# Kernel optimization log

Hardware: AMD Instinct MI355X
Metric: run time of the kernel (lower is better)

Reference implementation:

```python
import jax, jax.numpy as jnp
import numpy as np

EPS = 1e-8
N_CLASSES = 11


def _instance_loss(views_1, views_2, masks, labels):
    # views_*: [1, C, H, W]; masks: [1, K, H, W] binary; labels: [1, K] in [0,11)
    C = views_1.shape[1]
    X1 = views_1[0].reshape(C, -1)                      # [C, P]
    X2 = views_2[0].reshape(C, -1)                      # [C, P]
    K = masks.shape[1]
    M = (masks[0].reshape(K, -1) == 1).astype(X1.dtype) # [K, P]
    lab = labels[0]                                     # [K]

    counts = M.sum(axis=1)                              # [K] pixels per instance
    cnt = jnp.maximum(counts, 1.0)

    # per-instance mean feature vector over masked view-1 pixels
    per_chan_sum = M @ X1.T                             # [K, C]
    means = per_chan_sum / cnt[:, None]                 # [K, C]

    # torch.std over ALL elements of the gathered [N_k, C] block (unbiased)
    n_elem = counts * C                                 # [K]
    sum_all = per_chan_sum.sum(axis=1)                  # [K]
    mean_all = sum_all / jnp.maximum(n_elem, 1.0)
    sumsq = M @ (X1 * X1).sum(axis=0)                   # [K]
    var = (sumsq - n_elem * mean_all * mean_all) / jnp.maximum(n_elem - 1.0, 1.0)
    std = jnp.sqrt(jnp.maximum(var, 0.0))               # [K]

    # pairwise mean cosine sim: sim[i,j] = mean_{p in mask_j} cos(means[i], X2[:,p])
    norm_m = jnp.sqrt((means * means).sum(axis=1))      # [K]
    norm_2 = jnp.sqrt((X2 * X2).sum(axis=0))            # [P]
    D = means @ X2                                      # [K, P]
    ratio = D / jnp.maximum(norm_m[:, None] * norm_2[None, :], EPS)
    sim = (ratio @ M.T) / cnt[None, :]                  # [K, K]

    same = lab[:, None] == lab[None, :]
    eye = jnp.eye(K, dtype=bool)

    instance_sim = jnp.zeros(N_CLASSES, X1.dtype).at[lab].add(jnp.diagonal(sim))
    class_sim = jnp.zeros(N_CLASSES, X1.dtype).at[lab].add(
        jnp.where(same & ~eye, sim, 0.0).sum(axis=1))
    class_std = jnp.zeros(N_CLASSES, X1.dtype).at[lab].add(std)

    # negative-pair buckets: human={1,2}, 4wheel={3..8}, 2wheel={9,10}
    g_hum_4w = (lab >= 1) & (lab <= 8)                  # human or 4wheel
    g_4w_2w = (lab >= 3) & (lab <= 10)                  # 4wheel or 2wheel
    g_hum_2w = ((lab >= 1) & (lab <= 2)) | ((lab >= 9) & (lab <= 10))
    diff = ~same

    def neg_bucket(g):
        pair = diff & g[:, None] & g[None, :]
        c = pair.sum().astype(X1.dtype)
        s = jnp.where(pair, sim, 0.0).sum()
        return jnp.where(c > 1, s / c, s).reshape(1)

    neg_4w_hum = neg_bucket(g_hum_4w)
    neg_4w_2w = neg_bucket(g_4w_2w)
    neg_hum_2w = neg_bucket(g_hum_2w)

    class_counts = jnp.zeros(N_CLASSES, X1.dtype).at[lab].add(1.0)
    many = class_counts > 1
    instance_sim = jnp.where(many, instance_sim / jnp.maximum(class_counts, 1.0), instance_sim)
    class_sim = jnp.where(
        many, class_sim / jnp.maximum(class_counts * (class_counts - 1.0), 1.0), class_sim)
    class_std = jnp.where(many, class_std / jnp.maximum(class_counts, 1.0), class_std)

    return instance_sim, class_sim, neg_4w_hum, neg_4w_2w, neg_hum_2w, class_std


def setup_inputs() -> dict:
    key = jax.random.key(0)
    k1, k2, k3, k4 = jax.random.split(key, 4)
    views_1 = jax.random.normal(k1, (1, 64, 512, 512), dtype=jnp.float32)
    views_2 = jax.random.normal(k2, (1, 64, 512, 512), dtype=jnp.float32)
    masks = jax.random.randint(k3, (1, 16, 512, 512), 0, 2, dtype=jnp.int32)
    labels = jax.random.randint(k4, (1, 16), 0, 11, dtype=jnp.int32)
    return {"views_1": views_1, "views_2": views_2, "masks": masks, "labels": labels}


def reference(views_1, views_2, masks, labels):
    return _instance_loss(views_1, views_2, masks, labels)
```

## Files before the change

kernel.cpp:

```cpp
#include <hip/hip_runtime.h>

#define PIX 262144
#define CCH 64
#define KK  16

typedef __attribute__((ext_vector_type(8))) short short8;
typedef __attribute__((ext_vector_type(4))) float f32x4;

__device__ __forceinline__ float wred64(float v) {
    #pragma unroll
    for (int o = 32; o > 0; o >>= 1) v += __shfl_xor(v, o, 64);
    return v;
}

__global__ __launch_bounds__(256) void k2_all(
        const float* __restrict__ x1, const float* __restrict__ x2,
        const int* __restrict__ masks, float* __restrict__ counts_s,
        float* __restrict__ psum_c, float* __restrict__ psumsq_c,
        float* __restrict__ G_c) {
    __shared__ float ylds[128][4];
    int b = blockIdx.x;
    bool TB = (b >= 2048);
    if (TB) b -= 2048;
    int lane = threadIdx.x & 63;
    int wv   = threadIdx.x >> 6;
    int quad = lane >> 4;
    int n    = lane & 15;
    int ch   = wv * 16 + n;
    int base = b * 128;
    int cp   = b & 31;

    const float* Xrow = (TB ? x2 : x1) + (size_t)ch * PIX;
    const int*   Mrow = masks + (size_t)n * PIX;

    int4 mk[8]; float4 xa[4], xb[4];
    #pragma unroll
    for (int i = 0; i < 4; ++i) {
        int kof = base + i * 32 + (quad << 3);
        mk[2*i]   = *(const int4*)(Mrow + kof);
        mk[2*i+1] = *(const int4*)(Mrow + kof + 4);
        xa[i] = *(const float4*)(Xrow + kof);
        xb[i] = *(const float4*)(Xrow + kof + 4);
    }

    float xs[4][8], sq[4][8];
    #pragma unroll
    for (int i = 0; i < 4; ++i) {
        xs[i][0]=xa[i].x; xs[i][1]=xa[i].y; xs[i][2]=xa[i].z; xs[i][3]=xa[i].w;
        xs[i][4]=xb[i].x; xs[i][5]=xb[i].y; xs[i][6]=xb[i].z; xs[i][7]=xb[i].w;
        #pragma unroll
        for (int j = 0; j < 8; ++j) sq[i][j] = xs[i][j] * xs[i][j];
    }

    if (TB) {
        #pragma unroll
        for (int off = 1; off < 16; off <<= 1)
            #pragma unroll
            for (int i = 0; i < 4; ++i)
                #pragma unroll
                for (int j = 0; j < 8; ++j)
                    sq[i][j] += __shfl_xor(sq[i][j], off, 64);
        if (n == 0) {
            #pragma unroll
            for (int i = 0; i < 4; ++i)
                #pragma unroll
                for (int j = 0; j < 8; ++j)
                    ylds[i * 32 + (quad << 3) + j][wv] = sq[i][j];
        }
        __syncthreads();
        #pragma unroll
        for (int i = 0; i < 4; ++i)
            #pragma unroll
            for (int j = 0; j < 8; ++j) {
                float4 v = *(const float4*)ylds[i * 32 + (quad << 3) + j];
                float s = v.x + v.y + v.z + v.w;
                float y = (s > 0.f) ? rsqrtf(s) : 0.f;
                xs[i][j] *= y;
            }
    } else if (wv == 0) {
        int cnt = 0;
        #pragma unroll
        for (int i = 0; i < 8; ++i) {
            cnt += (mk[i].x == 1) + (mk[i].y == 1) + (mk[i].z == 1) + (mk[i].w == 1);
        }
        float fc = (float)cnt;
        fc += __shfl_xor(fc, 16, 64);
        fc += __shfl_xor(fc, 32, 64);
        if (quad == 0) atomicAdd(counts_s + n * 32 + cp, fc);
    }

    f32x4 acc0 = {0.f, 0.f, 0.f, 0.f};
    f32x4 acc1 = {0.f, 0.f, 0.f, 0.f};
    const short ONE = (short)0x3F80;

    #pragma unroll
    for (int i = 0; i < 4; ++i) {
        short8 af;
        af[0] = (mk[2*i].x   == 1) ? ONE : (short)0;
        af[1] = (mk[2*i].y   == 1) ? ONE : (short)0;
        af[2] = (mk[2*i].z   == 1) ? ONE : (short)0;
        af[3] = (mk[2*i].w   == 1) ? ONE : (short)0;
        af[4] = (mk[2*i+1].x == 1) ? ONE : (short)0;
        af[5] = (mk[2*i+1].y == 1) ? ONE : (short)0;
        af[6] = (mk[2*i+1].z == 1) ? ONE : (short)0;
        af[7] = (mk[2*i+1].w == 1) ? ONE : (short)0;

        short8 bh, bl;
        #pragma unroll
        for (int j = 0; j < 8; ++j) {
            float v = xs[i][j];
            unsigned u = __float_as_uint(v);
            bh[j] = (short)(u >> 16);
            float hi = __uint_as_float(u & 0xFFFF0000u);
            bl[j] = (short)(__float_as_uint(v - hi) >> 16);
        }
        acc0 = __builtin_amdgcn_mfma_f32_16x16x32_bf16(af, bh, acc0, 0, 0, 0);
        acc0 = __builtin_amdgcn_mfma_f32_16x16x32_bf16(af, bl, acc0, 0, 0, 0);

        if (!TB) {
            short8 qh, ql;
            #pragma unroll
            for (int j = 0; j < 8; ++j) {
                float v = sq[i][j];
                unsigned u = __float_as_uint(v);
                qh[j] = (short)(u >> 16);
                float hi = __uint_as_float(u & 0xFFFF0000u);
                ql[j] = (short)(__float_as_uint(v - hi) >> 16);
            }
            acc1 = __builtin_amdgcn_mfma_f32_16x16x32_bf16(af, qh, acc1, 0, 0, 0);
            acc1 = __builtin_amdgcn_mfma_f32_16x16x32_bf16(af, ql, acc1, 0, 0, 0);
        }
    }

    int col = wv * 16 + n;
    #pragma unroll
    for (int r = 0; r < 4; ++r) {
        int idx = cp * 1024 + (quad * 4 + r) * 64 + col;
        if (TB) {
            atomicAdd(G_c + idx, acc0[r]);
        } else {
            atomicAdd(psum_c + idx, acc0[r]);
            atomicAdd(psumsq_c + idx, acc1[r]);
        }
    }
}

__global__ __launch_bounds__(256) void k3_finalize(
        const int* __restrict__ labels, const float* __restrict__ counts_s,
        const float* __restrict__ psum_c, const float* __restrict__ psumsq_c,
        const float* __restrict__ G_c, float* __restrict__ out) {
    __shared__ float meansS[16][65];
    __shared__ float Gs[16][65];
    __shared__ float cntS[16], rawcS[16], nmS[16], stdS[16], rowS[16];
    __shared__ float ssq2[16][17];
    __shared__ float ssqS[16];
    __shared__ int   labS[16];
    __shared__ float simS[16][17];
    __shared__ float bred[4][6];
    int t = threadIdx.x;

    if (t < 16) {
        float s = 0.f;
        #pragma unroll 8
        for (int j = 0; j < 32; ++j) s += counts_s[t * 32 + j];
        rawcS[t] = s;
        cntS[t]  = fmaxf(s, 1.f);
        labS[t]  = labels[t];
    }
    {
        int k = t >> 4, seg = t & 15;
        float s = 0.f;
        for (int cp = 0; cp < 32; ++cp) {
            const float4 v = *(const float4*)(psumsq_c + cp * 1024 + k * 64 + seg * 4);
            s += v.x + v.y + v.z + v.w;
        }
        ssq2[k][seg] = s;
    }
    __syncthreads();
    if (t < 16) {
        float s = 0.f;
        #pragma unroll
        for (int seg = 0; seg < 16; ++seg) s += ssq2[t][seg];
        ssqS[t] = s;
    }
    for (int i = t; i < 1024; i += 256) {
        int k = i >> 6, c = i & 63;
        float sp = 0.f, sg = 0.f;
        #pragma unroll 8
        for (int cp = 0; cp < 32; ++cp) {
            sp += psum_c[cp * 1024 + i];
            sg += G_c[cp * 1024 + i];
        }
        meansS[k][c] = sp / cntS[k];
        Gs[k][c] = sg;
    }
    __syncthreads();
    if (t < 16) {
        float s2 = 0.f, sm = 0.f;
        for (int c = 0; c < 64; ++c) {
            float m = meansS[t][c];
            s2 = fmaf(m, m, s2);
            sm += m;
        }
        nmS[t] = sqrtf(s2);
        float ne = rawcS[t] * 64.f;
        float ma = (sm * cntS[t]) / fmaxf(ne, 1.f);
        float var = (ssqS[t] - ne * ma * ma) / fmaxf(ne - 1.f, 1.f);
        stdS[t] = sqrtf(fmaxf(var, 0.f));
    }
    __syncthreads();
    {
        int i = t >> 4, j = t & 15;
        float d = 0.f;
        #pragma unroll 16
        for (int c = 0; c < 64; ++c) d = fmaf(meansS[i][c], Gs[j][c], d);
        simS[i][j] = d / (fmaxf(nmS[i], 1e-30f) * cntS[j]);
    }
    __syncthreads();
    if (t < 16) {
        float s = 0.f;
        int li = labS[t];
        for (int j = 0; j < 16; ++j)
            if (j != t && labS[j] == li) s += simS[t][j];
        rowS[t] = s;
    }
    float s0 = 0.f, s1 = 0.f, s2 = 0.f, c0 = 0.f, c1 = 0.f, c2 = 0.f;
    {
        int i = t >> 4, j = t & 15;
        int li = labS[i], lj = labS[j];
        if (li != lj) {
            float sv = simS[i][j];
            bool gi0 = li >= 1 && li <= 8,  gj0 = lj >= 1 && lj <= 8;
            bool gi1 = li >= 3 && li <= 10, gj1 = lj >= 3 && lj <= 10;
            bool gi2 = (li >= 1 && li <= 2) || (li >= 9 && li <= 10);
            bool gj2 = (lj >= 1 && lj <= 2) || (lj >= 9 && lj <= 10);
            if (gi0 && gj0) { s0 = sv; c0 = 1.f; }
            if (gi1 && gj1) { s1 = sv; c1 = 1.f; }
            if (gi2 && gj2) { s2 = sv; c2 = 1.f; }
        }
    }
    s0 = wred64(s0); s1 = wred64(s1); s2 = wred64(s2);
    c0 = wred64(c0); c1 = wred64(c1); c2 = wred64(c2);
    {
        int wid = t >> 6, lane = t & 63;
        if (lane == 0) {
            bred[wid][0] = s0; bred[wid][1] = s1; bred[wid][2] = s2;
            bred[wid][3] = c0; bred[wid][4] = c1; bred[wid][5] = c2;
        }
    }
    __syncthreads();
    if (t < 11) {
        float cc = 0.f, inst = 0.f, csim = 0.f, cstd = 0.f;
        for (int k = 0; k < 16; ++k) {
            if (labS[k] == t) {
                cc += 1.f;
                inst += simS[k][k];
                csim += rowS[k];
                cstd += stdS[k];
            }
        }
        if (cc > 1.f) {
            inst /= fmaxf(cc, 1.f);
            csim /= fmaxf(cc * (cc - 1.f), 1.f);
            cstd /= cc;
        }
        out[t]      = inst;
        out[11 + t] = csim;
        out[25 + t] = cstd;
    }
    if (t == 0) {
        float S0 = bred[0][0] + bred[1][0] + bred[2][0] + bred[3][0];
        float S1 = bred[0][1] + bred[1][1] + bred[2][1] + bred[3][1];
        float S2 = bred[0][2] + bred[1][2] + bred[2][2] + bred[3][2];
        float C0 = bred[0][3] + bred[1][3] + bred[2][3] + bred[3][3];
        float C1 = bred[0][4] + bred[1][4] + bred[2][4] + bred[3][4];
        float C2 = bred[0][5] + bred[1][5] + bred[2][5] + bred[3][5];
        out[22] = (C0 > 1.f) ? (S0 / C0) : S0;
        out[23] = (C1 > 1.f) ? (S1 / C1) : S1;
        out[24] = (C2 > 1.f) ? (S2 / C2) : S2;
    }
}

extern "C" void kernel_launch(void* const* d_in, const int* in_sizes, int n_in,
                              void* d_out, int out_size, void* d_ws, size_t ws_size,
                              hipStream_t stream) {
    const float* x1     = (const float*)d_in[0];
    const float* x2     = (const float*)d_in[1];
    const int*   masks  = (const int*)d_in[2];
    const int*   labels = (const int*)d_in[3];
    float* out = (float*)d_out;

    float* ws = (float*)d_ws;
    float* counts_s = ws;
    float* psum_c   = counts_s + 512;
    float* psumsq_c = psum_c + 32 * 1024;
    float* G_c      = psumsq_c + 32 * 1024;

    hipMemsetAsync(counts_s, 0, (512 + 3 * 32 * 1024) * sizeof(float), stream);
    k2_all<<<4096, 256, 0, stream>>>(x1, x2, masks, counts_s, psum_c, psumsq_c, G_c);
    k3_finalize<<<1, 256, 0, stream>>>(labels, counts_s, psum_c, psumsq_c, G_c, out);
}
```

Measured before the change: 202.8 us.

## Coarsen pixel tiles per block and restructure x2 normalization to avoid LDS

Each block now handles 512 pixels instead of 128, which cuts the grid from 4096 to 1024 blocks and reduces the number of global atomics per output element. The view-1 path loops over four sub-chunks and merges the count computation into the main loop. The view-2 path has each wave own a pixel slice across all 64 channels, so the per-pixel norm is computed with in-wave shuffles and no LDS barrier. Per-wave partial products are then reduced through shared memory before a single atomic per element. The cost is more registers and less parallelism per block, since the loops run serially and there are fewer blocks in flight.

```diff
diff --git a/kernel.cpp b/kernel.cpp
--- a/kernel.cpp
+++ b/kernel.cpp
@@ -18,129 +18,165 @@
         const int* __restrict__ masks, float* __restrict__ counts_s,
         float* __restrict__ psum_c, float* __restrict__ psumsq_c,
         float* __restrict__ G_c) {
-    __shared__ float ylds[128][4];
-    int b = blockIdx.x;
-    bool TB = (b >= 2048);
-    if (TB) b -= 2048;
+    __shared__ float gl[4][1024];
     int lane = threadIdx.x & 63;
     int wv   = threadIdx.x >> 6;
     int quad = lane >> 4;
     int n    = lane & 15;
-    int ch   = wv * 16 + n;
-    int base = b * 128;
-    int cp   = b & 31;
-
-    const float* Xrow = (TB ? x2 : x1) + (size_t)ch * PIX;
-    const int*   Mrow = masks + (size_t)n * PIX;
-
-    int4 mk[8]; float4 xa[4], xb[4];
-    #pragma unroll
-    for (int i = 0; i < 4; ++i) {
-        int kof = base + i * 32 + (quad << 3);
-        mk[2*i]   = *(const int4*)(Mrow + kof);
-        mk[2*i+1] = *(const int4*)(Mrow + kof + 4);
-        xa[i] = *(const float4*)(Xrow + kof);
-        xb[i] = *(const float4*)(Xrow + kof + 4);
-    }
-
-    float xs[4][8], sq[4][8];
-    #pragma unroll
-    for (int i = 0; i < 4; ++i) {
-        xs[i][0]=xa[i].x; xs[i][1]=xa[i].y; xs[i][2]=xa[i].z; xs[i][3]=xa[i].w;
-        xs[i][4]=xb[i].x; xs[i][5]=xb[i].y; xs[i][6]=xb[i].z; xs[i][7]=xb[i].w;
+    const short ONE = (short)0x3F80;
+    const int* Mrow = masks + (size_t)n * PIX;
+
+    if (blockIdx.x < 512) {
+        int b = blockIdx.x;
+        int base = b * 512;
+        int cp   = b & 31;
+        const float* Xrow = x1 + (size_t)(wv * 16 + n) * PIX;
+
+        f32x4 acc0 = {0.f, 0.f, 0.f, 0.f};
+        f32x4 acc1 = {0.f, 0.f, 0.f, 0.f};
+        int cnt = 0;
+
+        for (int sc = 0; sc < 4; ++sc) {
+            int4 mk[8]; float4 xa[4], xb[4];
+            #pragma unroll
+            for (int i = 0; i < 4; ++i) {
+                int kof = base + sc * 128 + i * 32 + (quad << 3);
+                mk[2*i]   = *(const int4*)(Mrow + kof);
+                mk[2*i+1] = *(const int4*)(Mrow + kof + 4);
+                xa[i] = *(const float4*)(Xrow + kof);
+                xb[i] = *(const float4*)(Xrow + kof + 4);
+            }
+            #pragma unroll
+            for (int i = 0; i < 4; ++i) {
+                short8 af;
+                af[0] = (mk[2*i].x   == 1) ? ONE : (short)0;
+                af[1] = (mk[2*i].y   == 1) ? ONE : (short)0;
+                af[2] = (mk[2*i].z   == 1) ? ONE : (short)0;
+                af[3] = (mk[2*i].w   == 1) ? ONE : (short)0;
+                af[4] = (mk[2*i+1].x == 1) ? ONE : (short)0;
+                af[5] = (mk[2*i+1].y == 1) ? ONE : (short)0;
+                af[6] = (mk[2*i+1].z == 1) ? ONE : (short)0;
+                af[7] = (mk[2*i+1].w == 1) ? ONE : (short)0;
+                cnt += (mk[2*i].x == 1) + (mk[2*i].y == 1) + (mk[2*i].z == 1) + (mk[2*i].w == 1)
+                     + (mk[2*i+1].x == 1) + (mk[2*i+1].y == 1) + (mk[2*i+1].z == 1) + (mk[2*i+1].w == 1);
+
+                float xs[8] = {xa[i].x, xa[i].y, xa[i].z, xa[i].w,
+                               xb[i].x, xb[i].y, xb[i].z, xb[i].w};
+                short8 bh, bl, qh, ql;
+                #pragma unroll
+                for (int j = 0; j < 8; ++j) {
+                    float v = xs[j];
+                    unsigned u = __float_as_uint(v);
+                    bh[j] = (short)(u >> 16);
+                    float hi = __uint_as_float(u & 0xFFFF0000u);
+                    bl[j] = (short)(__float_as_uint(v - hi) >> 16);
+                    float sqv = v * v;
+                    unsigned uq = __float_as_uint(sqv);
+                    qh[j] = (short)(uq >> 16);
+                    float hq = __uint_as_float(uq & 0xFFFF0000u);
+                    ql[j] = (short)(__float_as_uint(sqv - hq) >> 16);
+                }
+                acc0 = __builtin_amdgcn_mfma_f32_16x16x32_bf16(af, bh, acc0, 0, 0, 0);
+                acc0 = __builtin_amdgcn_mfma_f32_16x16x32_bf16(af, bl, acc0, 0, 0, 0);
+                acc1 = __builtin_amdgcn_mfma_f32_16x16x32_bf16(af, qh, acc1, 0, 0, 0);
+                acc1 = __builtin_amdgcn_mfma_f32_16x16x32_bf16(af, ql, acc1, 0, 0, 0);
+            }
+        }
+
+        int col = wv * 16 + n;
         #pragma unroll
-        for (int j = 0; j < 8; ++j) sq[i][j] = xs[i][j] * xs[i][j];
-    }
-
-    if (TB) {
+        for (int r = 0; r < 4; ++r) {
+            int idx = cp * 1024 + (quad * 4 + r) * 64 + col;
+            atomicAdd(psum_c + idx, acc0[r]);
+            atomicAdd(psumsq_c + idx, acc1[r]);
+        }
+        if (wv == 0) {
+            float fc = (float)cnt;
+            fc += __shfl_xor(fc, 16, 64);
+            fc += __shfl_xor(fc, 32, 64);
+            if (quad == 0) atomicAdd(counts_s + n * 32 + cp, fc);
+        }
+    } else {
+        int b = blockIdx.x - 512;
+        int base = b * 512;
+        int cp   = b & 31;
+
+        f32x4 acc[4];
         #pragma unroll
-        for (int off = 1; off < 16; off <<= 1)
-            #pragma unroll
-            for (int i = 0; i < 4; ++i)
+        for (int cg = 0; cg < 4; ++cg) acc[cg] = (f32x4){0.f, 0.f, 0.f, 0.f};
+
+        for (int it = 0; it < 4; ++it) {
+            int pxo = base + it * 128 + wv * 32 + (quad << 3);
+            int4 mk0 = *(const int4*)(Mrow + pxo);
+            int4 mk1 = *(const int4*)(Mrow + pxo + 4);
+            float4 xla[4], xlb[4];
+            #pragma unroll
+            for (int cg = 0; cg < 4; ++cg) {
+                const float* Xr = x2 + (size_t)(cg * 16 + n) * PIX;
+                xla[cg] = *(const float4*)(Xr + pxo);
+                xlb[cg] = *(const float4*)(Xr + pxo + 4);
+            }
+
+            float xs[4][8];
+            #pragma unroll
+            for (int cg = 0; cg < 4; ++cg) {
+                xs[cg][0]=xla[cg].x; xs[cg][1]=xla[cg].y; xs[cg][2]=xla[cg].z; xs[cg][3]=xla[cg].w;
+                xs[cg][4]=xlb[cg].x; xs[cg][5]=xlb[cg].y; xs[cg][6]=xlb[cg].z; xs[cg][7]=xlb[cg].w;
+            }
+            float ss[8];
+            #pragma unroll
+            for (int j = 0; j < 8; ++j) {
+                float s = xs[0][j] * xs[0][j];
+                s = fmaf(xs[1][j], xs[1][j], s);
+                s = fmaf(xs[2][j], xs[2][j], s);
+                s = fmaf(xs[3][j], xs[3][j], s);
+                ss[j] = s;
+            }
+            #pragma unroll
+            for (int off = 1; off < 16; off <<= 1)
                 #pragma unroll
                 for (int j = 0; j < 8; ++j)
-                    sq[i][j] += __shfl_xor(sq[i][j], off, 64);
-        if (n == 0) {
-            #pragma unroll
-            for (int i = 0; i < 4; ++i)
+                    ss[j] += __shfl_xor(ss[j], off, 64);
+            float yw[8];
+            #pragma unroll
+            for (int j = 0; j < 8; ++j)
+                yw[j] = (ss[j] > 0.f) ? rsqrtf(ss[j]) : 0.f;
+
+            short8 af;
+            af[0] = (mk0.x == 1) ? ONE : (short)0;
+            af[1] = (mk0.y == 1) ? ONE : (short)0;
+            af[2] = (mk0.z == 1) ? ONE : (short)0;
+            af[3] = (mk0.w == 1) ? ONE : (short)0;
+            af[4] = (mk1.x == 1) ? ONE : (short)0;
+            af[5] = (mk1.y == 1) ? ONE : (short)0;
+            af[6] = (mk1.z == 1) ? ONE : (short)0;
+            af[7] = (mk1.w == 1) ? ONE : (short)0;
+
+            #pragma unroll
+            for (int cg = 0; cg < 4; ++cg) {
+                short8 bh, bl;
                 #pragma unroll
-                for (int j = 0; j < 8; ++j)
-                    ylds[i * 32 + (quad << 3) + j][wv] = sq[i][j];
-        }
+                for (int j = 0; j < 8; ++j) {
+                    float v = xs[cg][j] * yw[j];
+                    unsigned u = __float_as_uint(v);
+                    bh[j] = (short)(u >> 16);
+                    float hi = __uint_as_float(u & 0xFFFF0000u);
+                    bl[j] = (short)(__float_as_uint(v - hi) >> 16);
+                }
+                acc[cg] = __builtin_amdgcn_mfma_f32_16x16x32_bf16(af, bh, acc[cg], 0, 0, 0);
+                acc[cg] = __builtin_amdgcn_mfma_f32_16x16x32_bf16(af, bl, acc[cg], 0, 0, 0);
+            }
+        }
+
+        #pragma unroll
+        for (int cg = 0; cg < 4; ++cg)
+            #pragma unroll
+            for (int r = 0; r < 4; ++r)
+                gl[wv][(quad * 4 + r) * 64 + cg * 16 + n] = acc[cg][r];
         __syncthreads();
-        #pragma unroll
-        for (int i = 0; i < 4; ++i)
-            #pragma unroll
-            for (int j = 0; j < 8; ++j) {
-                float4 v = *(const float4*)ylds[i * 32 + (quad << 3) + j];
-                float s = v.x + v.y + v.z + v.w;
-                float y = (s > 0.f) ? rsqrtf(s) : 0.f;
-                xs[i][j] *= y;
-            }
-    } else if (wv == 0) {
-        int cnt = 0;
-        #pragma unroll
-        for (int i = 0; i < 8; ++i) {
-            cnt += (mk[i].x == 1) + (mk[i].y == 1) + (mk[i].z == 1) + (mk[i].w == 1);
-        }
-        float fc = (float)cnt;
-        fc += __shfl_xor(fc, 16, 64);
-        fc += __shfl_xor(fc, 32, 64);
-        if (quad == 0) atomicAdd(counts_s + n * 32 + cp, fc);
-    }
-
-    f32x4 acc0 = {0.f, 0.f, 0.f, 0.f};
-    f32x4 acc1 = {0.f, 0.f, 0.f, 0.f};
-    const short ONE = (short)0x3F80;
-
-    #pragma unroll
-    for (int i = 0; i < 4; ++i) {
-        short8 af;
-        af[0] = (mk[2*i].x   == 1) ? ONE : (short)0;
-        af[1] = (mk[2*i].y   == 1) ? ONE : (short)0;
-        af[2] = (mk[2*i].z   == 1) ? ONE : (short)0;
-        af[3] = (mk[2*i].w   == 1) ? ONE : (short)0;
-        af[4] = (mk[2*i+1].x == 1) ? ONE : (short)0;
-        af[5] = (mk[2*i+1].y == 1) ? ONE : (short)0;
-        af[6] = (mk[2*i+1].z == 1) ? ONE : (short)0;
-        af[7] = (mk[2*i+1].w == 1) ? ONE : (short)0;
-
-        short8 bh, bl;
-        #pragma unroll
-        for (int j = 0; j < 8; ++j) {
-            float v = xs[i][j];
-            unsigned u = __float_as_uint(v);
-            bh[j] = (short)(u >> 16);
-            float hi = __uint_as_float(u & 0xFFFF0000u);
-            bl[j] = (short)(__float_as_uint(v - hi) >> 16);
-        }
-        acc0 = __builtin_amdgcn_mfma_f32_16x16x32_bf16(af, bh, acc0, 0, 0, 0);
-        acc0 = __builtin_amdgcn_mfma_f32_16x16x32_bf16(af, bl, acc0, 0, 0, 0);
-
-        if (!TB) {
-            short8 qh, ql;
-            #pragma unroll
-            for (int j = 0; j < 8; ++j) {
-                float v = sq[i][j];
-                unsigned u = __float_as_uint(v);
-                qh[j] = (short)(u >> 16);
-                float hi = __uint_as_float(u & 0xFFFF0000u);
-                ql[j] = (short)(__float_as_uint(v - hi) >> 16);
-            }
-            acc1 = __builtin_amdgcn_mfma_f32_16x16x32_bf16(af, qh, acc1, 0, 0, 0);
-            acc1 = __builtin_amdgcn_mfma_f32_16x16x32_bf16(af, ql, acc1, 0, 0, 0);
-        }
-    }
-
-    int col = wv * 16 + n;
-    #pragma unroll
-    for (int r = 0; r < 4; ++r) {
-        int idx = cp * 1024 + (quad * 4 + r) * 64 + col;
-        if (TB) {
-            atomicAdd(G_c + idx, acc0[r]);
-        } else {
-            atomicAdd(psum_c + idx, acc0[r]);
-            atomicAdd(psumsq_c + idx, acc1[r]);
+        for (int e = threadIdx.x; e < 1024; e += 256) {
+            float s = gl[0][e] + gl[1][e] + gl[2][e] + gl[3][e];
+            atomicAdd(G_c + cp * 1024 + e, s);
         }
     }
 }
@@ -297,6 +333,6 @@
     float* G_c      = psumsq_c + 32 * 1024;
 
     hipMemsetAsync(counts_s, 0, (512 + 3 * 32 * 1024) * sizeof(float), stream);
-    k2_all<<<4096, 256, 0, stream>>>(x1, x2, masks, counts_s, psum_c, psumsq_c, G_c);
+    k2_all<<<1024, 256, 0, stream>>>(x1, x2, masks, counts_s, psum_c, psumsq_c, G_c);
     k3_finalize<<<1, 256, 0, stream>>>(labels, counts_s, psum_c, psumsq_c, G_c, out);
 }
```

Measured after the change: 188.6 us. -7.0%, faster.
